# Kernel optimization log

Measured on AMD Instinct MI355X. Metric: run time of the kernel, lower is better.

Reference implementation:

```python
import jax, jax.numpy as jnp
import numpy as np
import jax.scipy.linalg as jsl

# ---- module constants (mirror __init__ buffers) ----
T0, T1, DT = 0.0, 1.0, 1e-3
DIM, NSTEPS, M, TQ, B = 8, 2048, 64, 1024, 1
DS = (T1 - T0) / NSTEPS
STEPS = jnp.linspace(T0, T1, NSTEPS + 1)            # [S+1]
ZPTS = jnp.linspace(T0 + DT * 5.5, T1 - DT * 5.5, M)  # inducing points [M]
SQRT_DS = float(np.sqrt(DS))
SQRT_DT = float(np.sqrt(DT))


def _hurst(t, y0, W1, b1, W2, b2, Wc1, bc1, Wc2, bc2, dw, cw):
    # compute_hurst: sigmoid(driving_action(t)*dw + condition_net(y0)*cw)
    tc_in = t.reshape(-1, 1)                                             # [N,1]
    feat = jnp.concatenate([jnp.sin(tc_in), jnp.cos(tc_in), tc_in], -1)  # [N,3]
    tc = jax.nn.sigmoid(jnp.tanh(feat @ W1.T + b1) @ W2.T + b2)          # [N,dim]
    pc = jax.nn.sigmoid(jnp.tanh(y0 @ Wc1.T + bc1) @ Wc2.T + bc2)        # [1,dim]
    return jax.nn.sigmoid(tc * dw + pc * cw)                             # [N,dim]


def _safe_pow(x, a):
    # x**a for x>=0, with well-defined (zero) gradient at x==0
    mask = x > 0
    xs = jnp.where(mask, x, 1.0)
    return jnp.where(mask, xs ** a, 0.0)


def _compute_weight(t, y0, params, eps=1e-12):
    # compute_weight (Muniandy et al. weight); returns [S, N, dim]
    h = _hurst(t, y0, *params)[None]                              # [1,N,dim]
    d0 = jax.nn.relu(t[None, :] - STEPS[:-1, None])[..., None]    # [S,N,1]
    d1 = jax.nn.relu(t[None, :] - STEPS[1:, None])[..., None]     # [S,N,1]
    w = jnp.sqrt(_safe_pow(d0, 2.0 * h) - _safe_pow(d1, 2.0 * h) + eps)
    w = w / jnp.sqrt(2.0 * h * DS)
    return w / jnp.exp(jax.lax.lgamma(h + 0.5))


def _increment_weight(t, y0, params):
    # increment_weight: g_i / dt (finite difference of clamped weights)
    wa = jnp.maximum(_compute_weight(t, y0, params), 0.0)
    wb = jnp.maximum(_compute_weight(t + DT, y0, params), 0.0)
    return jnp.maximum((wb - wa) * SQRT_DS / DT, 0.0)             # [S,N,dim]


def _forward(t, y0, eps_z, W1, b1, W2, b2, Wc1, bc1, Wc2, bc2, dw, cw):
    params = (W1, b1, W2, b2, Wc1, bc1, Wc2, bc2, dw, cw)
    # --- precompute (inducing points) ---
    Kz = _increment_weight(ZPTS, y0, params)                # [S,M,dim]
    Kzz = jnp.einsum('smd,skd->dmk', Kz, Kz)                # [dim,M,M]
    Lz = jnp.linalg.cholesky(Kzz + 1e-6 * jnp.eye(M, dtype=Kzz.dtype))
    delta_Bz = jnp.einsum('dmk,dkb->dmb', Lz, eps_z)        # [dim,M,B]
    # --- forward (mean / sqrt(var)*sqrt(dt)) ---
    Kt = _increment_weight(t, y0, params)                   # [S,T,dim]
    Ktz = jnp.einsum('std,smd->dtm', Kt, Kz)                # [dim,T,M]
    alpha = jax.vmap(lambda L, b: jsl.cho_solve((L, True), b))(
        Lz, jnp.swapaxes(Ktz, -1, -2))                      # [dim,M,T]
    mean = jnp.einsum('dmt,dmb->dtb', alpha, delta_Bz)      # [dim,T,B]
    Ktt = jnp.einsum('std,sud->dtu', Kt, Kt)                # [dim,T,T]
    var = Ktt - jnp.einsum('dmt,dmu->dtu', alpha, alpha)    # [dim,T,T]
    std = jnp.sqrt(jnp.maximum(var, 1e-12)) * SQRT_DT
    return mean.reshape(-1, DIM), std.reshape(-1, DIM)


def setup_inputs() -> dict:
    key = jax.random.key(0)
    ks = jax.random.split(key, 12)
    return {
        't': jax.random.uniform(ks[0], (TQ,), jnp.float32, T0 + 0.05, T1 - 0.05),
        'y0': jax.random.normal(ks[1], (1, 1), jnp.float32),
        'eps_z': jax.random.normal(ks[2], (DIM, M, B), jnp.float32),
        'W1': jax.random.normal(ks[3], (10, 3), jnp.float32) * 0.3,
        'b1': jax.random.normal(ks[4], (10,), jnp.float32) * 0.1,
        'W2': jax.random.normal(ks[5], (DIM, 10), jnp.float32) * 0.3,
        'b2': jax.random.normal(ks[6], (DIM,), jnp.float32) * 0.1,
        'Wc1': jax.random.normal(ks[7], (10, 1), jnp.float32) * 0.3,
        'bc1': jax.random.normal(ks[8], (10,), jnp.float32) * 0.1,
        'Wc2': jax.random.normal(ks[9], (DIM, 10), jnp.float32) * 0.3,
        'bc2': jax.random.normal(ks[10], (DIM,), jnp.float32) * 0.1,
        'dw': jnp.array([0.5], jnp.float32),
        'cw': jnp.array([0.5], jnp.float32),
    }


def reference(t, y0, eps_z, W1, b1, W2, b2, Wc1, bc1, Wc2, bc2, dw, cw):
    return _forward(t, y0, eps_z, W1, b1, W2, b2, Wc1, bc1, Wc2, bc2, dw, cw)
```

## Files before the change

kernel.cpp:

```cpp
#include <hip/hip_runtime.h>
#include <cmath>

#define DIMN 8
#define SSTEPS 2048
#define MZ 64
#define TQN 1024
#define DS_F    4.8828125e-4f
#define DT_F    1.0e-3f
#define SCALE_F 22.09708691207961f
#define SQRTDT_F 0.031622776601683794f
#define LN2_F   0.6931471805599453f

typedef _Float16 f16x8 __attribute__((ext_vector_type(8)));
typedef float f32x4 __attribute__((ext_vector_type(4)));

__device__ __forceinline__ float sigmoidf_(float x) { return 1.f / (1.f + expf(-x)); }

__device__ __forceinline__ void gl_lds16(const _Float16* g, _Float16* l)
{
    __builtin_amdgcn_global_load_lds(
        (const __attribute__((address_space(1))) unsigned int*)g,
        (__attribute__((address_space(3))) unsigned int*)l, 16, 0, 0);
}

__global__ void coef_kernel(const float* __restrict__ t_in, const float* __restrict__ y0,
                            const float* __restrict__ W1, const float* __restrict__ b1,
                            const float* __restrict__ W2, const float* __restrict__ b2,
                            const float* __restrict__ Wc1, const float* __restrict__ bc1,
                            const float* __restrict__ Wc2, const float* __restrict__ bc2,
                            const float* __restrict__ dw, const float* __restrict__ cw,
                            float4* __restrict__ coef_t, float4* __restrict__ coef_z,
                            float* __restrict__ times_z)
{
    int gid = blockIdx.x * blockDim.x + threadIdx.x;
    if (gid >= TQN + MZ) return;
    bool isz = gid >= TQN;
    float tv;
    if (!isz) {
        tv = t_in[gid];
    } else {
        int j = gid - TQN;
        tv = 0.0055f + (float)j * (0.989f / 63.0f);
        times_z[j] = tv;
    }
    float y = y0[0];
    float hc[10];
    #pragma unroll
    for (int j = 0; j < 10; ++j) hc[j] = tanhf(y * Wc1[j] + bc1[j]);
    float pc[DIMN];
    #pragma unroll
    for (int d = 0; d < DIMN; ++d) {
        float s = bc2[d];
        #pragma unroll
        for (int j = 0; j < 10; ++j) s += hc[j] * Wc2[d * 10 + j];
        pc[d] = sigmoidf_(s);
    }
    float dww = dw[0], cww = cw[0];
    float4 outv[DIMN];
    for (int which = 0; which < 2; ++which) {
        float tt = (which == 0) ? tv : tv + DT_F;
        float st = sinf(tt), ct = cosf(tt);
        float hid[10];
        #pragma unroll
        for (int j = 0; j < 10; ++j)
            hid[j] = tanhf(st * W1[j * 3 + 0] + ct * W1[j * 3 + 1] + tt * W1[j * 3 + 2] + b1[j]);
        #pragma unroll
        for (int d = 0; d < DIMN; ++d) {
            float s = b2[d];
            #pragma unroll
            for (int j = 0; j < 10; ++j) s += hid[j] * W2[d * 10 + j];
            float tc = sigmoidf_(s);
            float h = sigmoidf_(tc * dww + pc[d] * cww);
            float e = 2.f * h;
            float c = rsqrtf(e * DS_F) / tgammaf(h + 0.5f);
            if (which == 0) { outv[d].x = e; outv[d].y = c; }
            else            { outv[d].z = e; outv[d].w = c; }
        }
    }
    float4* dst = isz ? (coef_z + (size_t)(gid - TQN) * DIMN) : (coef_t + (size_t)gid * DIMN);
    #pragma unroll
    for (int d = 0; d < DIMN; ++d) dst[d] = outv[d];
}

__device__ __forceinline__ void side_weights(float tt, float e, float c, int sbase,
                                             float (&w)[8])
{
    float xprev = tt - (float)sbase * DS_F;
    float pa = 0.f;
    if (xprev > 0.f) pa = __builtin_amdgcn_exp2f(e * __builtin_amdgcn_logf(xprev));
    #pragma unroll
    for (int k = 1; k <= 8; ++k) {
        float xk = tt - (float)(sbase + k) * DS_F;
        float D, pan;
        if (xk > 0.f) {
            float om = xk * __builtin_amdgcn_rcpf(xprev);
            float y2 = e * __builtin_amdgcn_logf(om);
            float wl = y2 * LN2_F;
            float em = wl * (1.f + wl * (0.5f + wl * (0.16666667f + wl * (0.041666668f + wl * 0.008333334f))));
            float g = -em;
            if (wl < -0.3f) g = 1.f - __builtin_amdgcn_exp2f(y2);
            D = pa * g;
            pan = pa - D;
        } else {
            D = pa;
            pan = 0.f;
        }
        w[k - 1] = __builtin_amdgcn_sqrtf(D + 1e-12f) * c;
        pa = pan;
        xprev = xk;
    }
}

__device__ __forceinline__ unsigned pack_hl(float v)
{
    _Float16 h = (_Float16)v;
    _Float16 l = (_Float16)(v - (float)h);
    unsigned short hu = __builtin_bit_cast(unsigned short, h);
    unsigned short lu = __builtin_bit_cast(unsigned short, l);
    return (unsigned)hu | ((unsigned)lu << 16);
}

__global__ __launch_bounds__(256) void kmat_t_kernel(const float* __restrict__ times,
                                                     const float4* __restrict__ coef,
                                                     _Float16* __restrict__ KThi,
                                                     _Float16* __restrict__ KTlo)
{
    int tid = threadIdx.x;
    int txx = tid & 31, sidx = tid >> 5;
    int t = blockIdx.x * 32 + txx;
    int sbase = blockIdx.y * 64 + sidx * 8;
    int d = blockIdx.z;
    __shared__ unsigned shhl[32][65];
    float tq = times[t];
    float4 cf = coef[(size_t)t * DIMN + d];
    float wa[8], wb[8];
    side_weights(tq,        cf.x, cf.y, sbase, wa);
    side_weights(tq + DT_F, cf.z, cf.w, sbase, wb);
    #pragma unroll
    for (int k = 0; k < 8; ++k) {
        float v = fmaxf(wb[k] - wa[k], 0.f) * SCALE_F;
        shhl[txx][sidx * 8 + k] = pack_hl(v);
    }
    __syncthreads();
    int tl = tid >> 3, sc = tid & 7;
    unsigned dwv[8];
    #pragma unroll
    for (int j = 0; j < 8; ++j) dwv[j] = shhl[tl][sc * 8 + j];
    uint4 hv, lv;
    hv.x = __builtin_amdgcn_perm(dwv[1], dwv[0], 0x05040100u);
    hv.y = __builtin_amdgcn_perm(dwv[3], dwv[2], 0x05040100u);
    hv.z = __builtin_amdgcn_perm(dwv[5], dwv[4], 0x05040100u);
    hv.w = __builtin_amdgcn_perm(dwv[7], dwv[6], 0x05040100u);
    lv.x = __builtin_amdgcn_perm(dwv[1], dwv[0], 0x07060302u);
    lv.y = __builtin_amdgcn_perm(dwv[3], dwv[2], 0x07060302u);
    lv.z = __builtin_amdgcn_perm(dwv[5], dwv[4], 0x07060302u);
    lv.w = __builtin_amdgcn_perm(dwv[7], dwv[6], 0x07060302u);
    size_t o = ((size_t)(d * 1024) + blockIdx.x * 32 + tl) * 2048 + blockIdx.y * 64 + sc * 8;
    *(uint4*)&KThi[o] = hv;
    *(uint4*)&KTlo[o] = lv;
}

__global__ __launch_bounds__(256) void kmat_z_kernel(const float* __restrict__ times,
                                                     const float4* __restrict__ coef,
                                                     float* __restrict__ Kz,
                                                     _Float16* __restrict__ KzThi,
                                                     _Float16* __restrict__ KzTlo)
{
    int tid = threadIdx.x;
    int txx = tid & 31, sidx = tid >> 5;
    int m = blockIdx.x * 32 + txx;
    int sbase = blockIdx.y * 64 + sidx * 8;
    int d = blockIdx.z;
    __shared__ unsigned shhl[32][65];
    float tq = times[m];
    float4 cf = coef[(size_t)m * DIMN + d];
    float wa[8], wb[8];
    side_weights(tq,        cf.x, cf.y, sbase, wa);
    side_weights(tq + DT_F, cf.z, cf.w, sbase, wb);
    #pragma unroll
    for (int k = 0; k < 8; ++k) {
        float v = fmaxf(wb[k] - wa[k], 0.f) * SCALE_F;
        Kz[((size_t)d * SSTEPS + sbase + k) * 64 + m] = v;
        shhl[txx][sidx * 8 + k] = pack_hl(v);
    }
    __syncthreads();
    int tl = tid >> 3, sc = tid & 7;
    unsigned dwv[8];
    #pragma unroll
    for (int j = 0; j < 8; ++j) dwv[j] = shhl[tl][sc * 8 + j];
    uint4 hv, lv;
    hv.x = __builtin_amdgcn_perm(dwv[1], dwv[0], 0x05040100u);
    hv.y = __builtin_amdgcn_perm(dwv[3], dwv[2], 0x05040100u);
    hv.z = __builtin_amdgcn_perm(dwv[5], dwv[4], 0x05040100u);
    hv.w = __builtin_amdgcn_perm(dwv[7], dwv[6], 0x05040100u);
    lv.x = __builtin_amdgcn_perm(dwv[1], dwv[0], 0x07060302u);
    lv.y = __builtin_amdgcn_perm(dwv[3], dwv[2], 0x07060302u);
    lv.z = __builtin_amdgcn_perm(dwv[5], dwv[4], 0x07060302u);
    lv.w = __builtin_amdgcn_perm(dwv[7], dwv[6], 0x07060302u);
    size_t o = ((size_t)(d * 64) + blockIdx.x * 32 + tl) * 2048 + blockIdx.y * 64 + sc * 8;
    *(uint4*)&KzThi[o] = hv;
    *(uint4*)&KzTlo[o] = lv;
}

__global__ __launch_bounds__(256) void kzz_partial_kernel(const float* __restrict__ Kz,
                                                          float* __restrict__ part)
{
    int kidx = blockIdx.x;
    int d = blockIdx.y;
    int tid = threadIdx.x, tx = tid & 15, ty = tid >> 4;
    __shared__ float As[32][64];
    float acc[4][4] = {};
    const float* base = Kz + ((size_t)d * SSTEPS + (size_t)kidx * 256) * 64;
    for (int c = 0; c < 8; ++c) {
        __syncthreads();
        #pragma unroll
        for (int l = 0; l < 2; ++l) {
            int idx = tid + l * 256;
            int r = idx >> 4, c4 = idx & 15;
            *(float4*)&As[r][c4 * 4] = *(const float4*)(base + (size_t)(c * 32 + r) * 64 + c4 * 4);
        }
        __syncthreads();
        #pragma unroll
        for (int k = 0; k < 32; ++k) {
            float av[4], bv[4];
            *(float4*)&av[0] = *(float4*)&As[k][ty * 4];
            *(float4*)&bv[0] = *(float4*)&As[k][tx * 4];
            #pragma unroll
            for (int i = 0; i < 4; ++i)
                #pragma unroll
                for (int j = 0; j < 4; ++j) acc[i][j] += av[i] * bv[j];
        }
    }
    float* dst = part + (size_t)(kidx * DIMN + d) * 4096;
    #pragma unroll
    for (int i = 0; i < 4; ++i)
        *(float4*)&dst[(size_t)(ty * 4 + i) * 64 + tx * 4] =
            make_float4(acc[i][0], acc[i][1], acc[i][2], acc[i][3]);
}

__global__ void reduce_kernel(const float* __restrict__ in, float* __restrict__ out,
                              int n, int parts)
{
    int i = blockIdx.x * 256 + threadIdx.x;
    if (i >= n) return;
    float s = 0.f;
    for (int p = 0; p < parts; ++p) s += in[(size_t)p * n + i];
    out[i] = s;
}

__global__ __launch_bounds__(64) void chol_kernel(const float* __restrict__ Kzz,
                                                  const float* __restrict__ eps_z,
                                                  float* __restrict__ Lz, float* __restrict__ dBz)
{
    int d = blockIdx.x, i = threadIdx.x;
    __shared__ float A[64][65];
    for (int r = 0; r < 64; ++r)
        A[r][i] = Kzz[(size_t)d * 4096 + (size_t)r * 64 + i] + ((r == i) ? 1e-6f : 0.f);
    __syncthreads();
    for (int j = 0; j < 64; ++j) {
        float s = 0.f;
        if (i >= j) {
            s = A[i][j];
            for (int k = 0; k < j; ++k) s -= A[i][k] * A[j][k];
        }
        __syncthreads();
        if (i == j) A[j][j] = sqrtf(fmaxf(s, 1e-30f));
        __syncthreads();
        if (i > j) A[i][j] = s / A[j][j];
        __syncthreads();
    }
    for (int r = 0; r < 64; ++r)
        Lz[(size_t)d * 4096 + (size_t)r * 64 + i] = (i <= r) ? A[r][i] : 0.f;
    float s = 0.f;
    for (int k = 0; k <= i; ++k) s += A[i][k] * eps_z[d * 64 + k];
    dBz[d * 64 + i] = s;
}

__global__ __launch_bounds__(256, 2) void ktz_mfma_kernel(const _Float16* __restrict__ KThi,
                                                          const _Float16* __restrict__ KTlo,
                                                          const _Float16* __restrict__ KzThi,
                                                          const _Float16* __restrict__ KzTlo,
                                                          float* __restrict__ part)
{
    int tid = threadIdx.x;
    int wave = tid >> 6, lane = tid & 63;
    int n = lane & 15, q = lane >> 4;
    int lr = lane >> 2, lc = (lane & 3) * 8;
    int d = blockIdx.x;
    int t0 = blockIdx.y * 128;
    int split = blockIdx.z;
    int wr = (wave >> 1) * 64, wc = (wave & 1) * 32;

    __shared__ _Float16 Ah[2][128][32], Al[2][128][32];
    __shared__ _Float16 Bh[2][64][32],  Bl[2][64][32];

    f32x4 acc[4][2];
    #pragma unroll
    for (int i = 0; i < 4; ++i)
        #pragma unroll
        for (int j = 0; j < 2; ++j) acc[i][j] = (f32x4)0.f;

    const size_t aRow = (size_t)(d * 1024 + t0);
    const size_t bRow = (size_t)(d * 64);
    int segA = wave * 32;
    int segB = wave * 16;

    auto stage = [&](int buf, int c) {
        int s0 = split * 512 + c * 32;
        size_t ga = (aRow + segA + lr) * 2048 + s0 + lc;
        size_t gb = (bRow + segB + lr) * 2048 + s0 + lc;
        gl_lds16(KThi + ga,               &Ah[buf][segA][0]);
        gl_lds16(KThi + ga + 16 * 2048,   &Ah[buf][segA + 16][0]);
        gl_lds16(KTlo + ga,               &Al[buf][segA][0]);
        gl_lds16(KTlo + ga + 16 * 2048,   &Al[buf][segA + 16][0]);
        gl_lds16(KzThi + gb,              &Bh[buf][segB][0]);
        gl_lds16(KzTlo + gb,              &Bl[buf][segB][0]);
    };

    stage(0, 0);
    for (int c = 0; c < 16; ++c) {
        int buf = c & 1;
        asm volatile("s_waitcnt vmcnt(0)" ::: "memory");
        __builtin_amdgcn_s_barrier();
        __builtin_amdgcn_sched_barrier(0);
        if (c + 1 < 16) stage(buf ^ 1, c + 1);
        f16x8 fAh[4], fAl[4], fBh[2], fBl[2];
        #pragma unroll
        for (int i = 0; i < 4; ++i) {
            fAh[i] = *(f16x8*)&Ah[buf][wr + i * 16 + n][q * 8];
            fAl[i] = *(f16x8*)&Al[buf][wr + i * 16 + n][q * 8];
        }
        #pragma unroll
        for (int j = 0; j < 2; ++j) {
            fBh[j] = *(f16x8*)&Bh[buf][wc + j * 16 + n][q * 8];
            fBl[j] = *(f16x8*)&Bl[buf][wc + j * 16 + n][q * 8];
        }
        asm volatile("s_waitcnt lgkmcnt(0)" ::: "memory");
        __builtin_amdgcn_sched_barrier(0);
        __builtin_amdgcn_s_setprio(1);
        #pragma unroll
        for (int i = 0; i < 4; ++i)
            #pragma unroll
            for (int j = 0; j < 2; ++j) {
                acc[i][j] = __builtin_amdgcn_mfma_f32_16x16x32_f16(fAh[i], fBh[j], acc[i][j], 0, 0, 0);
                acc[i][j] = __builtin_amdgcn_mfma_f32_16x16x32_f16(fAh[i], fBl[j], acc[i][j], 0, 0, 0);
                acc[i][j] = __builtin_amdgcn_mfma_f32_16x16x32_f16(fAl[i], fBh[j], acc[i][j], 0, 0, 0);
            }
        __builtin_amdgcn_s_setprio(0);
    }
    float* dst = part + ((size_t)(split * DIMN + d)) * 1024 * 64;
    #pragma unroll
    for (int i = 0; i < 4; ++i)
        #pragma unroll
        for (int j = 0; j < 2; ++j)
            #pragma unroll
            for (int r = 0; r < 4; ++r) {
                int t = t0 + wr + i * 16 + q * 4 + r;
                dst[(size_t)t * 64 + wc + j * 16 + n] = acc[i][j][r];
            }
}

__global__ __launch_bounds__(64) void solve_kernel(const float* __restrict__ Lz,
                                                   const float* __restrict__ part2,
                                                   const float* __restrict__ dBz,
                                                   _Float16* __restrict__ aPhi,
                                                   _Float16* __restrict__ aPlo,
                                                   _Float16* __restrict__ aNhi,
                                                   _Float16* __restrict__ aNlo,
                                                   float* __restrict__ out0)
{
    int d = blockIdx.y;
    int t0 = blockIdx.x * 64;
    int i = threadIdx.x;
    __shared__ float L[64][65];
    __shared__ float bL[64][65];
    __shared__ float inv[64];
    __shared__ float dB[64];
    for (int r = 0; r < 64; ++r)
        L[r][i] = Lz[(size_t)d * 4096 + (size_t)r * 64 + i];
    dB[i] = dBz[d * 64 + i];
    for (int r = 0; r < 64; ++r) {
        size_t base = ((size_t)d * 1024 + t0 + r) * 64 + i;
        float s = part2[base] + part2[base + 524288] + part2[base + 1048576] + part2[base + 1572864];
        bL[i][r] = s;
    }
    __syncthreads();
    inv[i] = 1.f / L[i][i];
    __syncthreads();
    for (int j = 0; j < 64; ++j) {
        float s = bL[j][i];
        for (int k = 0; k < j; ++k) s -= L[j][k] * bL[k][i];
        bL[j][i] = s * inv[j];
    }
    for (int j = 63; j >= 0; --j) {
        float s = bL[j][i];
        for (int k = j + 1; k < 64; ++k) s -= L[k][j] * bL[k][i];
        bL[j][i] = s * inv[j];
    }
    float mn = 0.f;
    for (int m = 0; m < 64; ++m) mn += bL[m][i] * dB[m];
    out0[d * 1024 + t0 + i] = mn;
    size_t o = ((size_t)(d * 1024 + t0 + i)) * 64;
    for (int g = 0; g < 8; ++g) {
        union { _Float16 h[8]; float4 v; } ph, pl, nh, nl;
        #pragma unroll
        for (int k = 0; k < 8; ++k) {
            float x = bL[g * 8 + k][i];
            _Float16 h = (_Float16)x;
            _Float16 lo = (_Float16)(x - (float)h);
            ph.h[k] = h;  pl.h[k] = lo;
            nh.h[k] = -h; nl.h[k] = -lo;
        }
        *(float4*)&aPhi[o + g * 8] = ph.v;
        *(float4*)&aPlo[o + g * 8] = pl.v;
        *(float4*)&aNhi[o + g * 8] = nh.v;
        *(float4*)&aNlo[o + g * 8] = nl.v;
    }
}

__global__ __launch_bounds__(256, 3) void var_mfma_kernel(const _Float16* __restrict__ KThi,
                                                          const _Float16* __restrict__ KTlo,
                                                          const _Float16* __restrict__ aPhi,
                                                          const _Float16* __restrict__ aPlo,
                                                          const _Float16* __restrict__ aNhi,
                                                          const _Float16* __restrict__ aNlo,
                                                          float* __restrict__ out1)
{
    int tid = threadIdx.x;
    int wave = tid >> 6, lane = tid & 63;
    int n = lane & 15, q = lane >> 4;
    int lr = lane >> 2;
    int lcs = (((lane & 3) ^ ((lr >> 1) & 3)) * 8);
    int qs  = ((q ^ ((n >> 1) & 3)) * 8);
    int d = blockIdx.x;
    int ti = 0, rem = blockIdx.y;
    while (rem >= 16 - 2 * ti) { rem -= 16 - 2 * ti; ++ti; }
    int uj = 2 * ti + rem;
    int t0 = ti * 128, u0 = uj * 64;
    int wr = (wave >> 1) * 64, wc = (wave & 1) * 32;

    __shared__ _Float16 Ah[2][128][32], Al[2][128][32];
    __shared__ _Float16 Bh[2][64][32],  Bl[2][64][32];

    f32x4 acc[4][2];
    #pragma unroll
    for (int i = 0; i < 4; ++i)
        #pragma unroll
        for (int j = 0; j < 2; ++j) acc[i][j] = (f32x4)0.f;

    const size_t aRow = (size_t)(d * 1024 + t0);
    const size_t bRow = (size_t)(d * 1024 + u0);
    int sa = wave * 32;
    int sb = wave * 16;

    auto stage = [&](int buf, int ck) {
        const _Float16 *ph, *pl, *qh, *ql;
        size_t str; int col;
        if (ck < 64) { ph = KThi; pl = KTlo; qh = KThi; ql = KTlo; str = 2048; col = ck * 32; }
        else         { ph = aPhi; pl = aPlo; qh = aNhi; ql = aNlo; str = 64;  col = (ck - 64) * 32; }
        size_t ga = (aRow + sa + lr) * str + col + lcs;
        size_t gb = (bRow + sb + lr) * str + col + lcs;
        gl_lds16(ph + ga,            &Ah[buf][sa][0]);
        gl_lds16(ph + ga + 16 * str, &Ah[buf][sa + 16][0]);
        gl_lds16(pl + ga,            &Al[buf][sa][0]);
        gl_lds16(pl + ga + 16 * str, &Al[buf][sa + 16][0]);
        gl_lds16(qh + gb,            &Bh[buf][sb][0]);
        gl_lds16(ql + gb,            &Bl[buf][sb][0]);
    };

    stage(0, 0);
    for (int ck = 0; ck < 66; ++ck) {
        int buf = ck & 1;
        asm volatile("s_waitcnt vmcnt(0)" ::: "memory");
        __builtin_amdgcn_s_barrier();
        __builtin_amdgcn_sched_barrier(0);
        if (ck + 1 < 66) stage(buf ^ 1, ck + 1);
        f16x8 fAh[4], fAl[4], fBh[2], fBl[2];
        #pragma unroll
        for (int i = 0; i < 4; ++i) {
            fAh[i] = *(f16x8*)&Ah[buf][wr + i * 16 + n][qs];
            fAl[i] = *(f16x8*)&Al[buf][wr + i * 16 + n][qs];
        }
        #pragma unroll
        for (int j = 0; j < 2; ++j) {
            fBh[j] = *(f16x8*)&Bh[buf][wc + j * 16 + n][qs];
            fBl[j] = *(f16x8*)&Bl[buf][wc + j * 16 + n][qs];
        }
        asm volatile("s_waitcnt lgkmcnt(0)" ::: "memory");
        __builtin_amdgcn_sched_barrier(0);
        __builtin_amdgcn_s_setprio(1);
        #pragma unroll
        for (int i = 0; i < 4; ++i)
            #pragma unroll
            for (int j = 0; j < 2; ++j) {
                acc[i][j] = __builtin_amdgcn_mfma_f32_16x16x32_f16(fAh[i], fBh[j], acc[i][j], 0, 0, 0);
                acc[i][j] = __builtin_amdgcn_mfma_f32_16x16x32_f16(fAh[i], fBl[j], acc[i][j], 0, 0, 0);
                acc[i][j] = __builtin_amdgcn_mfma_f32_16x16x32_f16(fAl[i], fBh[j], acc[i][j], 0, 0, 0);
            }
        __builtin_amdgcn_s_setprio(0);
    }
    float* dst = out1 + ((size_t)d << 20);
    int tw0 = t0 + wr;
    int uw0 = u0 + wc;
    bool above = (uw0 >= tw0 + 64);
    bool below = (uw0 + 32 <= tw0);
    if (!below) {
        #pragma unroll
        for (int i = 0; i < 4; ++i) {
            int tb = tw0 + i * 16 + q * 4;
            #pragma unroll
            for (int j = 0; j < 2; ++j) {
                int u = uw0 + j * 16 + n;
                float fv[4];
                #pragma unroll
                for (int r = 0; r < 4; ++r)
                    fv[r] = sqrtf(fmaxf(acc[i][j][r], 1e-12f)) * SQRTDT_F;
                if (above) {
                    #pragma unroll
                    for (int r = 0; r < 4; ++r)
                        dst[(size_t)(tb + r) * 1024 + u] = fv[r];
                    *(float4*)&dst[(size_t)u * 1024 + tb] = make_float4(fv[0], fv[1], fv[2], fv[3]);
                } else {
                    #pragma unroll
                    for (int r = 0; r < 4; ++r) {
                        int t = tb + r;
                        if (u >= t) dst[(size_t)t * 1024 + u] = fv[r];
                        if (u > t)  dst[(size_t)u * 1024 + t] = fv[r];
                    }
                }
            }
        }
    }
}

extern "C" void kernel_launch(void* const* d_in, const int* in_sizes, int n_in,
                              void* d_out, int out_size, void* d_ws, size_t ws_size,
                              hipStream_t stream)
{
    const float* t_in  = (const float*)d_in[0];
    const float* y0    = (const float*)d_in[1];
    const float* eps_z = (const float*)d_in[2];
    const float* W1    = (const float*)d_in[3];
    const float* b1    = (const float*)d_in[4];
    const float* W2    = (const float*)d_in[5];
    const float* b2    = (const float*)d_in[6];
    const float* Wc1   = (const float*)d_in[7];
    const float* bc1   = (const float*)d_in[8];
    const float* Wc2   = (const float*)d_in[9];
    const float* bc2   = (const float*)d_in[10];
    const float* dw    = (const float*)d_in[11];
    const float* cw    = (const float*)d_in[12];

    float* ws = (float*)d_ws;
    size_t off = 0;
    auto carve = [&](size_t n) { float* p = ws + off; off += n; return p; };
    float* coef_t   = carve(32768);
    float* coef_z   = carve(2048);
    float* times_z  = carve(64);
    float* Kzz      = carve(32768);
    float* Lz       = carve(32768);
    float* dBz      = carve(512);
    float* Kz       = carve(1048576);
    _Float16* KThi  = (_Float16*)carve(8388608);
    _Float16* KTlo  = (_Float16*)carve(8388608);
    _Float16* KzThi = (_Float16*)carve(524288);
    _Float16* KzTlo = (_Float16*)carve(524288);
    float* part1    = carve(262144);
    float* part2    = carve(2097152);
    _Float16* aPhi  = (_Float16*)carve(262144);
    _Float16* aPlo  = (_Float16*)carve(262144);
    _Float16* aNhi  = (_Float16*)carve(262144);
    _Float16* aNlo  = (_Float16*)carve(262144);

    float* out0 = (float*)d_out;
    float* out1 = out0 + (size_t)DIMN * 1024;

    coef_kernel<<<9, 128, 0, stream>>>(t_in, y0, W1, b1, W2, b2, Wc1, bc1, Wc2, bc2, dw, cw,
                                       (float4*)coef_t, (float4*)coef_z, times_z);
    kmat_t_kernel<<<dim3(32, 32, 8), 256, 0, stream>>>(t_in, (const float4*)coef_t,
                                                       KThi, KTlo);
    kmat_z_kernel<<<dim3(2, 32, 8), 256, 0, stream>>>(times_z, (const float4*)coef_z,
                                                      Kz, KzThi, KzTlo);
    kzz_partial_kernel<<<dim3(8, 8), 256, 0, stream>>>(Kz, part1);
    reduce_kernel<<<128, 256, 0, stream>>>(part1, Kzz, 32768, 8);
    chol_kernel<<<8, 64, 0, stream>>>(Kzz, eps_z, Lz, dBz);
    ktz_mfma_kernel<<<dim3(8, 8, 4), 256, 0, stream>>>(KThi, KTlo, KzThi, KzTlo, part2);
    solve_kernel<<<dim3(16, 8), 64, 0, stream>>>(Lz, part2, dBz, aPhi, aPlo, aNhi, aNlo, out0);
    var_mfma_kernel<<<dim3(8, 72), 256, 0, stream>>>(KThi, KTlo, aPhi, aPlo, aNhi, aNlo, out1);
}
```

Measured before the change: 365.1 us.

## Shrink MFMA tiles to 64x64, swizzle ktz LDS, fold Kzz reduce into Cholesky

The partial-sum reduction kernel is removed and the eight Kzz partials are summed directly when the Cholesky kernel loads its matrix, saving one launch. The ktz and var MFMA kernels drop from 128x64 to 64x64 output tiles, which doubles the block count to fill more CUs. It also raises the occupancy hint to 4. The ktz kernel gains the XOR-swizzled LDS addressing that var already used, to cut bank conflicts. Smaller tiles lower data reuse per loaded byte, and the triangular var grid now carries more diagonal tiles with partial writes.

```diff
diff --git a/kernel.cpp b/kernel.cpp
--- a/kernel.cpp
+++ b/kernel.cpp
@@ -238,24 +238,19 @@
             make_float4(acc[i][0], acc[i][1], acc[i][2], acc[i][3]);
 }
 
-__global__ void reduce_kernel(const float* __restrict__ in, float* __restrict__ out,
-                              int n, int parts)
-{
-    int i = blockIdx.x * 256 + threadIdx.x;
-    if (i >= n) return;
-    float s = 0.f;
-    for (int p = 0; p < parts; ++p) s += in[(size_t)p * n + i];
-    out[i] = s;
-}
-
-__global__ __launch_bounds__(64) void chol_kernel(const float* __restrict__ Kzz,
+__global__ __launch_bounds__(64) void chol_kernel(const float* __restrict__ part1,
                                                   const float* __restrict__ eps_z,
                                                   float* __restrict__ Lz, float* __restrict__ dBz)
 {
     int d = blockIdx.x, i = threadIdx.x;
     __shared__ float A[64][65];
-    for (int r = 0; r < 64; ++r)
-        A[r][i] = Kzz[(size_t)d * 4096 + (size_t)r * 64 + i] + ((r == i) ? 1e-6f : 0.f);
+    for (int r = 0; r < 64; ++r) {
+        size_t base = (size_t)d * 4096 + (size_t)r * 64 + i;
+        float s = 0.f;
+        #pragma unroll
+        for (int p = 0; p < 8; ++p) s += part1[base + (size_t)p * 32768];
+        A[r][i] = s + ((r == i) ? 1e-6f : 0.f);
+    }
     __syncthreads();
     for (int j = 0; j < 64; ++j) {
         float s = 0.f;
@@ -276,7 +271,7 @@
     dBz[d * 64 + i] = s;
 }
 
-__global__ __launch_bounds__(256, 2) void ktz_mfma_kernel(const _Float16* __restrict__ KThi,
+__global__ __launch_bounds__(256, 4) void ktz_mfma_kernel(const _Float16* __restrict__ KThi,
                                                           const _Float16* __restrict__ KTlo,
                                                           const _Float16* __restrict__ KzThi,
                                                           const _Float16* __restrict__ KzTlo,
@@ -285,36 +280,35 @@
     int tid = threadIdx.x;
     int wave = tid >> 6, lane = tid & 63;
     int n = lane & 15, q = lane >> 4;
-    int lr = lane >> 2, lc = (lane & 3) * 8;
+    int lr = lane >> 2;
+    int lcs = (((lane & 3) ^ ((lr >> 1) & 3)) * 8);
+    int qs  = ((q ^ ((n >> 1) & 3)) * 8);
     int d = blockIdx.x;
-    int t0 = blockIdx.y * 128;
+    int t0 = blockIdx.y * 64;
     int split = blockIdx.z;
-    int wr = (wave >> 1) * 64, wc = (wave & 1) * 32;
-
-    __shared__ _Float16 Ah[2][128][32], Al[2][128][32];
-    __shared__ _Float16 Bh[2][64][32],  Bl[2][64][32];
-
-    f32x4 acc[4][2];
-    #pragma unroll
-    for (int i = 0; i < 4; ++i)
+    int wr = (wave >> 1) * 32, wc = (wave & 1) * 32;
+
+    __shared__ _Float16 Ah[2][64][32], Al[2][64][32];
+    __shared__ _Float16 Bh[2][64][32], Bl[2][64][32];
+
+    f32x4 acc[2][2];
+    #pragma unroll
+    for (int i = 0; i < 2; ++i)
         #pragma unroll
         for (int j = 0; j < 2; ++j) acc[i][j] = (f32x4)0.f;
 
     const size_t aRow = (size_t)(d * 1024 + t0);
     const size_t bRow = (size_t)(d * 64);
-    int segA = wave * 32;
-    int segB = wave * 16;
+    int sr = wave * 16;
 
     auto stage = [&](int buf, int c) {
         int s0 = split * 512 + c * 32;
-        size_t ga = (aRow + segA + lr) * 2048 + s0 + lc;
-        size_t gb = (bRow + segB + lr) * 2048 + s0 + lc;
-        gl_lds16(KThi + ga,               &Ah[buf][segA][0]);
-        gl_lds16(KThi + ga + 16 * 2048,   &Ah[buf][segA + 16][0]);
-        gl_lds16(KTlo + ga,               &Al[buf][segA][0]);
-        gl_lds16(KTlo + ga + 16 * 2048,   &Al[buf][segA + 16][0]);
-        gl_lds16(KzThi + gb,              &Bh[buf][segB][0]);
-        gl_lds16(KzTlo + gb,              &Bl[buf][segB][0]);
+        size_t ga = (aRow + sr + lr) * 2048 + s0 + lcs;
+        size_t gb = (bRow + sr + lr) * 2048 + s0 + lcs;
+        gl_lds16(KThi + ga,  &Ah[buf][sr][0]);
+        gl_lds16(KTlo + ga,  &Al[buf][sr][0]);
+        gl_lds16(KzThi + gb, &Bh[buf][sr][0]);
+        gl_lds16(KzTlo + gb, &Bl[buf][sr][0]);
     };
 
     stage(0, 0);
@@ -324,22 +318,19 @@
         __builtin_amdgcn_s_barrier();
         __builtin_amdgcn_sched_barrier(0);
         if (c + 1 < 16) stage(buf ^ 1, c + 1);
-        f16x8 fAh[4], fAl[4], fBh[2], fBl[2];
-        #pragma unroll
-        for (int i = 0; i < 4; ++i) {
-            fAh[i] = *(f16x8*)&Ah[buf][wr + i * 16 + n][q * 8];
-            fAl[i] = *(f16x8*)&Al[buf][wr + i * 16 + n][q * 8];
-        }
-        #pragma unroll
-        for (int j = 0; j < 2; ++j) {
-            fBh[j] = *(f16x8*)&Bh[buf][wc + j * 16 + n][q * 8];
-            fBl[j] = *(f16x8*)&Bl[buf][wc + j * 16 + n][q * 8];
+        f16x8 fAh[2], fAl[2], fBh[2], fBl[2];
+        #pragma unroll
+        for (int i = 0; i < 2; ++i) {
+            fAh[i] = *(f16x8*)&Ah[buf][wr + i * 16 + n][qs];
+            fAl[i] = *(f16x8*)&Al[buf][wr + i * 16 + n][qs];
+            fBh[i] = *(f16x8*)&Bh[buf][wc + i * 16 + n][qs];
+            fBl[i] = *(f16x8*)&Bl[buf][wc + i * 16 + n][qs];
         }
         asm volatile("s_waitcnt lgkmcnt(0)" ::: "memory");
         __builtin_amdgcn_sched_barrier(0);
         __builtin_amdgcn_s_setprio(1);
         #pragma unroll
-        for (int i = 0; i < 4; ++i)
+        for (int i = 0; i < 2; ++i)
             #pragma unroll
             for (int j = 0; j < 2; ++j) {
                 acc[i][j] = __builtin_amdgcn_mfma_f32_16x16x32_f16(fAh[i], fBh[j], acc[i][j], 0, 0, 0);
@@ -350,7 +341,7 @@
     }
     float* dst = part + ((size_t)(split * DIMN + d)) * 1024 * 64;
     #pragma unroll
-    for (int i = 0; i < 4; ++i)
+    for (int i = 0; i < 2; ++i)
         #pragma unroll
         for (int j = 0; j < 2; ++j)
             #pragma unroll
@@ -418,7 +409,7 @@
     }
 }
 
-__global__ __launch_bounds__(256, 3) void var_mfma_kernel(const _Float16* __restrict__ KThi,
+__global__ __launch_bounds__(256, 4) void var_mfma_kernel(const _Float16* __restrict__ KThi,
                                                           const _Float16* __restrict__ KTlo,
                                                           const _Float16* __restrict__ aPhi,
                                                           const _Float16* __restrict__ aPlo,
@@ -434,38 +425,35 @@
     int qs  = ((q ^ ((n >> 1) & 3)) * 8);
     int d = blockIdx.x;
     int ti = 0, rem = blockIdx.y;
-    while (rem >= 16 - 2 * ti) { rem -= 16 - 2 * ti; ++ti; }
-    int uj = 2 * ti + rem;
-    int t0 = ti * 128, u0 = uj * 64;
-    int wr = (wave >> 1) * 64, wc = (wave & 1) * 32;
-
-    __shared__ _Float16 Ah[2][128][32], Al[2][128][32];
-    __shared__ _Float16 Bh[2][64][32],  Bl[2][64][32];
-
-    f32x4 acc[4][2];
-    #pragma unroll
-    for (int i = 0; i < 4; ++i)
+    while (rem >= 16 - ti) { rem -= 16 - ti; ++ti; }
+    int uj = ti + rem;
+    int t0 = ti * 64, u0 = uj * 64;
+    int wr = (wave >> 1) * 32, wc = (wave & 1) * 32;
+
+    __shared__ _Float16 Ah[2][64][32], Al[2][64][32];
+    __shared__ _Float16 Bh[2][64][32], Bl[2][64][32];
+
+    f32x4 acc[2][2];
+    #pragma unroll
+    for (int i = 0; i < 2; ++i)
         #pragma unroll
         for (int j = 0; j < 2; ++j) acc[i][j] = (f32x4)0.f;
 
     const size_t aRow = (size_t)(d * 1024 + t0);
     const size_t bRow = (size_t)(d * 1024 + u0);
-    int sa = wave * 32;
-    int sb = wave * 16;
+    int sr = wave * 16;
 
     auto stage = [&](int buf, int ck) {
         const _Float16 *ph, *pl, *qh, *ql;
         size_t str; int col;
         if (ck < 64) { ph = KThi; pl = KTlo; qh = KThi; ql = KTlo; str = 2048; col = ck * 32; }
         else         { ph = aPhi; pl = aPlo; qh = aNhi; ql = aNlo; str = 64;  col = (ck - 64) * 32; }
-        size_t ga = (aRow + sa + lr) * str + col + lcs;
-        size_t gb = (bRow + sb + lr) * str + col + lcs;
-        gl_lds16(ph + ga,            &Ah[buf][sa][0]);
-        gl_lds16(ph + ga + 16 * str, &Ah[buf][sa + 16][0]);
-        gl_lds16(pl + ga,            &Al[buf][sa][0]);
-        gl_lds16(pl + ga + 16 * str, &Al[buf][sa + 16][0]);
-        gl_lds16(qh + gb,            &Bh[buf][sb][0]);
-        gl_lds16(ql + gb,            &Bl[buf][sb][0]);
+        size_t ga = (aRow + sr + lr) * str + col + lcs;
+        size_t gb = (bRow + sr + lr) * str + col + lcs;
+        gl_lds16(ph + ga, &Ah[buf][sr][0]);
+        gl_lds16(pl + ga, &Al[buf][sr][0]);
+        gl_lds16(qh + gb, &Bh[buf][sr][0]);
+        gl_lds16(ql + gb, &Bl[buf][sr][0]);
     };
 
     stage(0, 0);
@@ -475,22 +463,19 @@
         __builtin_amdgcn_s_barrier();
         __builtin_amdgcn_sched_barrier(0);
         if (ck + 1 < 66) stage(buf ^ 1, ck + 1);
-        f16x8 fAh[4], fAl[4], fBh[2], fBl[2];
-        #pragma unroll
-        for (int i = 0; i < 4; ++i) {
+        f16x8 fAh[2], fAl[2], fBh[2], fBl[2];
+        #pragma unroll
+        for (int i = 0; i < 2; ++i) {
             fAh[i] = *(f16x8*)&Ah[buf][wr + i * 16 + n][qs];
             fAl[i] = *(f16x8*)&Al[buf][wr + i * 16 + n][qs];
-        }
-        #pragma unroll
-        for (int j = 0; j < 2; ++j) {
-            fBh[j] = *(f16x8*)&Bh[buf][wc + j * 16 + n][qs];
-            fBl[j] = *(f16x8*)&Bl[buf][wc + j * 16 + n][qs];
+            fBh[i] = *(f16x8*)&Bh[buf][wc + i * 16 + n][qs];
+            fBl[i] = *(f16x8*)&Bl[buf][wc + i * 16 + n][qs];
         }
         asm volatile("s_waitcnt lgkmcnt(0)" ::: "memory");
         __builtin_amdgcn_sched_barrier(0);
         __builtin_amdgcn_s_setprio(1);
         #pragma unroll
-        for (int i = 0; i < 4; ++i)
+        for (int i = 0; i < 2; ++i)
             #pragma unroll
             for (int j = 0; j < 2; ++j) {
                 acc[i][j] = __builtin_amdgcn_mfma_f32_16x16x32_f16(fAh[i], fBh[j], acc[i][j], 0, 0, 0);
@@ -502,11 +487,11 @@
     float* dst = out1 + ((size_t)d << 20);
     int tw0 = t0 + wr;
     int uw0 = u0 + wc;
-    bool above = (uw0 >= tw0 + 64);
+    bool above = (uw0 >= tw0 + 32);
     bool below = (uw0 + 32 <= tw0);
     if (!below) {
         #pragma unroll
-        for (int i = 0; i < 4; ++i) {
+        for (int i = 0; i < 2; ++i) {
             int tb = tw0 + i * 16 + q * 4;
             #pragma unroll
             for (int j = 0; j < 2; ++j) {
@@ -571,6 +556,7 @@
     _Float16* aPlo  = (_Float16*)carve(262144);
     _Float16* aNhi  = (_Float16*)carve(262144);
     _Float16* aNlo  = (_Float16*)carve(262144);
+    (void)Kzz;
 
     float* out0 = (float*)d_out;
     float* out1 = out0 + (size_t)DIMN * 1024;
@@ -582,9 +568,8 @@
     kmat_z_kernel<<<dim3(2, 32, 8), 256, 0, stream>>>(times_z, (const float4*)coef_z,
                                                       Kz, KzThi, KzTlo);
     kzz_partial_kernel<<<dim3(8, 8), 256, 0, stream>>>(Kz, part1);
-    reduce_kernel<<<128, 256, 0, stream>>>(part1, Kzz, 32768, 8);
-    chol_kernel<<<8, 64, 0, stream>>>(Kzz, eps_z, Lz, dBz);
-    ktz_mfma_kernel<<<dim3(8, 8, 4), 256, 0, stream>>>(KThi, KTlo, KzThi, KzTlo, part2);
+    chol_kernel<<<8, 64, 0, stream>>>(part1, eps_z, Lz, dBz);
+    ktz_mfma_kernel<<<dim3(8, 16, 4), 256, 0, stream>>>(KThi, KTlo, KzThi, KzTlo, part2);
     solve_kernel<<<dim3(16, 8), 64, 0, stream>>>(Lz, part2, dBz, aPhi, aPlo, aNhi, aNlo, out0);
-    var_mfma_kernel<<<dim3(8, 72), 256, 0, stream>>>(KThi, KTlo, aPhi, aPlo, aNhi, aNlo, out1);
-}
+    var_mfma_kernel<<<dim3(8, 136), 256, 0, stream>>>(KThi, KTlo, aPhi, aPlo, aNhi, aNlo, out1);
+}
```

Result: slower. 401.3 us (+9.9%).

## Sort query times and skip zero causal-weight chunks in kmat and matmul kernels

Applied to the files above, without the earlier changes.

Adds a single-block bitonic sort of the query times, producing sorted times plus forward and inverse permutations. Rows of the weight matrix are then built in sorted order. kmat_t, ktz_mfma and var_mfma skip step blocks or K-chunks that lie past a band's largest time plus a margin, since the relu-based weights are zero there. Outputs are scattered back through the permutation, and a new colperm kernel reorders the columns of every variance row. It also drops the explicit lgkmcnt waits before the MFMA loops. The cost is extra launches plus a full read and write of the 8×1024×1024 output for the column permutation.

```diff
diff --git a/kernel.cpp b/kernel.cpp
--- a/kernel.cpp
+++ b/kernel.cpp
@@ -80,6 +80,40 @@
     float4* dst = isz ? (coef_z + (size_t)(gid - TQN) * DIMN) : (coef_t + (size_t)gid * DIMN);
     #pragma unroll
     for (int d = 0; d < DIMN; ++d) dst[d] = outv[d];
+}
+
+__global__ __launch_bounds__(512) void sort_kernel(const float* __restrict__ t_in,
+                                                   float* __restrict__ tsort,
+                                                   int* __restrict__ perm,
+                                                   int* __restrict__ inv)
+{
+    __shared__ float v[1024];
+    __shared__ int   ix[1024];
+    int tid = threadIdx.x;
+    v[tid] = t_in[tid];             ix[tid] = tid;
+    v[tid + 512] = t_in[tid + 512]; ix[tid + 512] = tid + 512;
+    __syncthreads();
+    for (int k = 2; k <= 1024; k <<= 1) {
+        for (int j = k >> 1; j > 0; j >>= 1) {
+            #pragma unroll 1
+            for (int base = 0; base < 1024; base += 512) {
+                int i = base + tid;
+                int p = i ^ j;
+                if (p > i) {
+                    bool up = ((i & k) == 0);
+                    float vi = v[i], vp = v[p];
+                    if ((vi > vp) == up) {
+                        v[i] = vp; v[p] = vi;
+                        int q_ = ix[i]; ix[i] = ix[p]; ix[p] = q_;
+                    }
+                }
+            }
+            __syncthreads();
+        }
+    }
+    tsort[tid] = v[tid];           tsort[tid + 512] = v[tid + 512];
+    perm[tid] = ix[tid];           perm[tid + 512] = ix[tid + 512];
+    inv[ix[tid]] = tid;            inv[ix[tid + 512]] = tid + 512;
 }
 
 __device__ __forceinline__ void side_weights(float tt, float e, float c, int sbase,
@@ -120,19 +154,23 @@
     return (unsigned)hu | ((unsigned)lu << 16);
 }
 
-__global__ __launch_bounds__(256) void kmat_t_kernel(const float* __restrict__ times,
+__global__ __launch_bounds__(256) void kmat_t_kernel(const float* __restrict__ tsort,
+                                                     const int* __restrict__ perm,
                                                      const float4* __restrict__ coef,
                                                      _Float16* __restrict__ KThi,
                                                      _Float16* __restrict__ KTlo)
 {
+    int band = blockIdx.x >> 2;
+    float bmax = tsort[band * 128 + 127];
+    if ((float)(blockIdx.y * 64) * DS_F > bmax + DT_F + 0.07f) return;
     int tid = threadIdx.x;
     int txx = tid & 31, sidx = tid >> 5;
     int t = blockIdx.x * 32 + txx;
     int sbase = blockIdx.y * 64 + sidx * 8;
     int d = blockIdx.z;
     __shared__ unsigned shhl[32][65];
-    float tq = times[t];
-    float4 cf = coef[(size_t)t * DIMN + d];
+    float tq = tsort[t];
+    float4 cf = coef[(size_t)perm[t] * DIMN + d];
     float wa[8], wb[8];
     side_weights(tq,        cf.x, cf.y, sbase, wa);
     side_weights(tq + DT_F, cf.z, cf.w, sbase, wb);
@@ -280,6 +318,7 @@
                                                           const _Float16* __restrict__ KTlo,
                                                           const _Float16* __restrict__ KzThi,
                                                           const _Float16* __restrict__ KzTlo,
+                                                          const float* __restrict__ tsort,
                                                           float* __restrict__ part)
 {
     int tid = threadIdx.x;
@@ -290,6 +329,11 @@
     int t0 = blockIdx.y * 128;
     int split = blockIdx.z;
     int wr = (wave >> 1) * 64, wc = (wave & 1) * 32;
+
+    float tmax = tsort[t0 + 127];
+    int klim = (int)floorf((tmax + DT_F) * 64.f) + 2;
+    int nc = klim - split * 16;
+    nc = nc < 0 ? 0 : (nc > 16 ? 16 : nc);
 
     __shared__ _Float16 Ah[2][128][32], Al[2][128][32];
     __shared__ _Float16 Bh[2][64][32],  Bl[2][64][32];
@@ -317,13 +361,13 @@
         gl_lds16(KzTlo + gb,              &Bl[buf][segB][0]);
     };
 
-    stage(0, 0);
-    for (int c = 0; c < 16; ++c) {
+    if (nc > 0) stage(0, 0);
+    for (int c = 0; c < nc; ++c) {
         int buf = c & 1;
         asm volatile("s_waitcnt vmcnt(0)" ::: "memory");
         __builtin_amdgcn_s_barrier();
         __builtin_amdgcn_sched_barrier(0);
-        if (c + 1 < 16) stage(buf ^ 1, c + 1);
+        if (c + 1 < nc) stage(buf ^ 1, c + 1);
         f16x8 fAh[4], fAl[4], fBh[2], fBl[2];
         #pragma unroll
         for (int i = 0; i < 4; ++i) {
@@ -335,8 +379,6 @@
             fBh[j] = *(f16x8*)&Bh[buf][wc + j * 16 + n][q * 8];
             fBl[j] = *(f16x8*)&Bl[buf][wc + j * 16 + n][q * 8];
         }
-        asm volatile("s_waitcnt lgkmcnt(0)" ::: "memory");
-        __builtin_amdgcn_sched_barrier(0);
         __builtin_amdgcn_s_setprio(1);
         #pragma unroll
         for (int i = 0; i < 4; ++i)
@@ -363,6 +405,7 @@
 __global__ __launch_bounds__(64) void solve_kernel(const float* __restrict__ Lz,
                                                    const float* __restrict__ part2,
                                                    const float* __restrict__ dBz,
+                                                   const int* __restrict__ perm,
                                                    _Float16* __restrict__ aPhi,
                                                    _Float16* __restrict__ aPlo,
                                                    _Float16* __restrict__ aNhi,
@@ -399,7 +442,7 @@
     }
     float mn = 0.f;
     for (int m = 0; m < 64; ++m) mn += bL[m][i] * dB[m];
-    out0[d * 1024 + t0 + i] = mn;
+    out0[d * 1024 + perm[t0 + i]] = mn;
     size_t o = ((size_t)(d * 1024 + t0 + i)) * 64;
     for (int g = 0; g < 8; ++g) {
         union { _Float16 h[8]; float4 v; } ph, pl, nh, nl;
@@ -424,6 +467,8 @@
                                                           const _Float16* __restrict__ aPlo,
                                                           const _Float16* __restrict__ aNhi,
                                                           const _Float16* __restrict__ aNlo,
+                                                          const float* __restrict__ tsort,
+                                                          const int* __restrict__ perm,
                                                           float* __restrict__ out1)
 {
     int tid = threadIdx.x;
@@ -438,6 +483,12 @@
     int uj = 2 * ti + rem;
     int t0 = ti * 128, u0 = uj * 64;
     int wr = (wave >> 1) * 64, wc = (wave & 1) * 32;
+
+    float tmaxv = tsort[t0 + 127];
+    float umaxv = tsort[u0 + 63];
+    int nck = (int)floorf((fminf(tmaxv, umaxv) + DT_F) * 64.f) + 2;
+    if (nck > 64) nck = 64;
+    int nit = nck + 2;
 
     __shared__ _Float16 Ah[2][128][32], Al[2][128][32];
     __shared__ _Float16 Bh[2][64][32],  Bl[2][64][32];
@@ -469,12 +520,13 @@
     };
 
     stage(0, 0);
-    for (int ck = 0; ck < 66; ++ck) {
-        int buf = ck & 1;
+    for (int it = 0; it < nit; ++it) {
+        int buf = it & 1;
         asm volatile("s_waitcnt vmcnt(0)" ::: "memory");
         __builtin_amdgcn_s_barrier();
         __builtin_amdgcn_sched_barrier(0);
-        if (ck + 1 < 66) stage(buf ^ 1, ck + 1);
+        int nx = it + 1;
+        if (nx < nit) stage(buf ^ 1, nx < nck ? nx : 64 + (nx - nck));
         f16x8 fAh[4], fAl[4], fBh[2], fBl[2];
         #pragma unroll
         for (int i = 0; i < 4; ++i) {
@@ -486,8 +538,6 @@
             fBh[j] = *(f16x8*)&Bh[buf][wc + j * 16 + n][qs];
             fBl[j] = *(f16x8*)&Bl[buf][wc + j * 16 + n][qs];
         }
-        asm volatile("s_waitcnt lgkmcnt(0)" ::: "memory");
-        __builtin_amdgcn_sched_barrier(0);
         __builtin_amdgcn_s_setprio(1);
         #pragma unroll
         for (int i = 0; i < 4; ++i)
@@ -511,6 +561,7 @@
             #pragma unroll
             for (int j = 0; j < 2; ++j) {
                 int u = uw0 + j * 16 + n;
+                int pu = perm[u];
                 float fv[4];
                 #pragma unroll
                 for (int r = 0; r < 4; ++r)
@@ -518,18 +569,34 @@
                 if (above) {
                     #pragma unroll
                     for (int r = 0; r < 4; ++r)
-                        dst[(size_t)(tb + r) * 1024 + u] = fv[r];
-                    *(float4*)&dst[(size_t)u * 1024 + tb] = make_float4(fv[0], fv[1], fv[2], fv[3]);
+                        dst[(size_t)perm[tb + r] * 1024 + u] = fv[r];
+                    *(float4*)&dst[(size_t)pu * 1024 + tb] = make_float4(fv[0], fv[1], fv[2], fv[3]);
                 } else {
                     #pragma unroll
                     for (int r = 0; r < 4; ++r) {
                         int t = tb + r;
-                        if (u >= t) dst[(size_t)t * 1024 + u] = fv[r];
-                        if (u > t)  dst[(size_t)u * 1024 + t] = fv[r];
+                        if (u >= t) dst[(size_t)perm[t] * 1024 + u] = fv[r];
+                        if (u > t)  dst[(size_t)pu * 1024 + t] = fv[r];
                     }
                 }
             }
         }
+    }
+}
+
+__global__ __launch_bounds__(256) void colperm_kernel(float* __restrict__ out1,
+                                                      const int* __restrict__ invp)
+{
+    int d = blockIdx.y, row = blockIdx.x;
+    float* rp = out1 + ((size_t)d << 20) + (size_t)row * 1024;
+    __shared__ float buf[1024];
+    int tid = threadIdx.x;
+    *(float4*)&buf[tid * 4] = *(float4*)&rp[tid * 4];
+    __syncthreads();
+    #pragma unroll
+    for (int k = 0; k < 4; ++k) {
+        int b = tid + k * 256;
+        rp[b] = buf[invp[b]];
     }
 }
 
@@ -571,20 +638,27 @@
     _Float16* aPlo  = (_Float16*)carve(262144);
     _Float16* aNhi  = (_Float16*)carve(262144);
     _Float16* aNlo  = (_Float16*)carve(262144);
+    float* tsort    = carve(1024);
+    int*   perm_i   = (int*)carve(1024);
+    int*   inv_i    = (int*)carve(1024);
 
     float* out0 = (float*)d_out;
     float* out1 = out0 + (size_t)DIMN * 1024;
 
     coef_kernel<<<9, 128, 0, stream>>>(t_in, y0, W1, b1, W2, b2, Wc1, bc1, Wc2, bc2, dw, cw,
                                        (float4*)coef_t, (float4*)coef_z, times_z);
-    kmat_t_kernel<<<dim3(32, 32, 8), 256, 0, stream>>>(t_in, (const float4*)coef_t,
+    sort_kernel<<<1, 512, 0, stream>>>(t_in, tsort, perm_i, inv_i);
+    kmat_t_kernel<<<dim3(32, 32, 8), 256, 0, stream>>>(tsort, perm_i, (const float4*)coef_t,
                                                        KThi, KTlo);
     kmat_z_kernel<<<dim3(2, 32, 8), 256, 0, stream>>>(times_z, (const float4*)coef_z,
                                                       Kz, KzThi, KzTlo);
     kzz_partial_kernel<<<dim3(8, 8), 256, 0, stream>>>(Kz, part1);
     reduce_kernel<<<128, 256, 0, stream>>>(part1, Kzz, 32768, 8);
     chol_kernel<<<8, 64, 0, stream>>>(Kzz, eps_z, Lz, dBz);
-    ktz_mfma_kernel<<<dim3(8, 8, 4), 256, 0, stream>>>(KThi, KTlo, KzThi, KzTlo, part2);
-    solve_kernel<<<dim3(16, 8), 64, 0, stream>>>(Lz, part2, dBz, aPhi, aPlo, aNhi, aNlo, out0);
-    var_mfma_kernel<<<dim3(8, 72), 256, 0, stream>>>(KThi, KTlo, aPhi, aPlo, aNhi, aNlo, out1);
-}
+    ktz_mfma_kernel<<<dim3(8, 8, 4), 256, 0, stream>>>(KThi, KTlo, KzThi, KzTlo, tsort, part2);
+    solve_kernel<<<dim3(16, 8), 64, 0, stream>>>(Lz, part2, dBz, perm_i,
+                                                 aPhi, aPlo, aNhi, aNlo, out0);
+    var_mfma_kernel<<<dim3(8, 72), 256, 0, stream>>>(KThi, KTlo, aPhi, aPlo, aNhi, aNlo,
+                                                     tsort, perm_i, out1);
+    colperm_kernel<<<dim3(1024, 8), 256, 0, stream>>>(out1, inv_i);
+}
```

Measured after the change: 381.5 us. +4.5%, slower.
